# Optimization experiments

Measured on AMD Instinct MI355X. Metric: run time of the kernel, lower is better.

Reference implementation:

```python
import jax, jax.numpy as jnp
import numpy as np

NUM_EXPERTS = 8
TOP_K = 2


def setup_inputs() -> dict:
    key = jax.random.key(0)
    ks = jax.random.split(key, 5)
    B, S, H, F, E = 2, 2048, 1024, 4096, NUM_EXPERTS
    return {
        "hidden_states": jax.random.normal(ks[0], (B, S, H), dtype=jnp.float32),
        "router_w": jax.random.normal(ks[1], (H, E), dtype=jnp.float32) * 0.02,
        "router_b": jnp.zeros((E,), dtype=jnp.float32),
        "w1": jax.random.normal(ks[2], (E, H, F), dtype=jnp.float32) * 0.02,
        "b1": jnp.zeros((E, F), dtype=jnp.float32),
        "w2": jax.random.normal(ks[3], (E, F, H), dtype=jnp.float32) * 0.02,
        "b2": jnp.zeros((E, H), dtype=jnp.float32),
    }


def reference(hidden_states, router_w, router_b, w1, b1, w2, b2):
    # Router: softmax over experts, take top-2, renormalize.
    logits = jnp.einsum("bsh,he->bse", hidden_states, router_w) + router_b
    probs = jax.nn.softmax(logits, axis=-1)
    top_w, top_i = jax.lax.top_k(probs, TOP_K)              # [B,S,2]
    top_w = top_w / jnp.sum(top_w, axis=-1, keepdims=True)
    # Combine weights per expert: [B,S,E] (sum of slot weights where routed).
    combine = jnp.sum(
        top_w[..., None] * jax.nn.one_hot(top_i, NUM_EXPERTS, dtype=top_w.dtype),
        axis=-2,
    )
    # Dense expert FFN over stacked experts (grouped GEMM form).
    h = jax.nn.gelu(
        jnp.einsum("bsh,ehf->ebsf", hidden_states, w1) + b1[:, None, None, :],
        approximate=False,
    )  # exact GELU matches torch nn.GELU default
    y = jnp.einsum("ebsf,efh->ebsh", h, w2) + b2[:, None, None, :]
    # Weighted combine of top-2 expert outputs per token.
    return jnp.einsum("bse,ebsh->bsh", combine, y)
```

## Files before the change

kernel.cpp:

```cpp
#include <hip/hip_runtime.h>
#include <hip/hip_bf16.h>
#include <stdint.h>

#define T_TOKENS 4096
#define H_DIM    1024
#define F_DIM    4096
#define NE       8
#define NA       8192

typedef __bf16 bf16x8 __attribute__((ext_vector_type(8)));
typedef float  f32x4  __attribute__((ext_vector_type(4)));

__device__ __forceinline__ float b2f(unsigned short u) {
    union { float f; uint32_t i; } v; v.i = ((uint32_t)u) << 16; return v.f;
}
__device__ __forceinline__ unsigned short f2b(float f) {
    union { float f; uint32_t i; } v; v.f = f;
    uint32_t x = v.i;
    return (unsigned short)((x + 0x7FFFu + ((x >> 16) & 1u)) >> 16);
}

__device__ __forceinline__ void gl_lds16(const void* g, void* l) {
    __builtin_amdgcn_global_load_lds(
        (const __attribute__((address_space(1))) void*)g,
        (__attribute__((address_space(3))) void*)l,
        16, 0, 0);
}

__global__ void probe_kernel(const unsigned short* __restrict__ hs,
                             int* __restrict__ flag) {
    int lane = threadIdx.x;
    int cnt = 0;
    for (int j = 0; j < 16; j++) {
        unsigned short u = hs[(lane * 16 + j) * 2];
        int e = (u >> 7) & 0xFF;
        if (e >= 100 && e <= 135) cnt++;
    }
    for (int off = 32; off > 0; off >>= 1) cnt += __shfl_down(cnt, off);
    if (lane == 0) *flag = (cnt >= 512) ? 0 : 1;
}

__global__ __launch_bounds__(256) void router_kernel(
    const void* __restrict__ hs, const void* __restrict__ rw,
    const void* __restrict__ rb, const int* __restrict__ flag,
    int* __restrict__ top_i, float* __restrict__ top_w,
    unsigned short* __restrict__ hsb) {
    bool f32 = (*flag != 0);
    int wave = threadIdx.x >> 6, lane = threadIdx.x & 63;
    int t = blockIdx.x * 4 + wave;
    unsigned short* hout = hsb + (size_t)t * H_DIM;
    float acc[NE];
#pragma unroll
    for (int e = 0; e < NE; e++) acc[e] = 0.f;
    if (f32) {
        const float* hrow = (const float*)hs + (size_t)t * H_DIM;
        const float* rwf = (const float*)rw;
        for (int j = 0; j < 16; j++) {
            int k = j * 64 + lane;
            float h = hrow[k];
            hout[k] = f2b(h);
            float4 a = *(const float4*)(rwf + (size_t)k * NE);
            float4 b = *(const float4*)(rwf + (size_t)k * NE + 4);
            acc[0] += h * a.x; acc[1] += h * a.y; acc[2] += h * a.z; acc[3] += h * a.w;
            acc[4] += h * b.x; acc[5] += h * b.y; acc[6] += h * b.z; acc[7] += h * b.w;
        }
    } else {
        const unsigned short* hrow = (const unsigned short*)hs + (size_t)t * H_DIM;
        const unsigned short* rwu = (const unsigned short*)rw;
        for (int j = 0; j < 16; j++) {
            int k = j * 64 + lane;
            unsigned short hu = hrow[k];
            hout[k] = hu;
            float h = b2f(hu);
            uint4 rv = *(const uint4*)(rwu + (size_t)k * NE);
            const unsigned short* rs = (const unsigned short*)&rv;
#pragma unroll
            for (int e = 0; e < NE; e++) acc[e] += h * b2f(rs[e]);
        }
    }
#pragma unroll
    for (int e = 0; e < NE; e++)
        for (int off = 32; off > 0; off >>= 1) acc[e] += __shfl_down(acc[e], off);
    if (lane == 0) {
        float lg[NE];
#pragma unroll
        for (int e = 0; e < NE; e++)
            lg[e] = acc[e] + (f32 ? ((const float*)rb)[e]
                                  : b2f(((const unsigned short*)rb)[e]));
        int e0 = 0;
        for (int e = 1; e < NE; e++) if (lg[e] > lg[e0]) e0 = e;
        int e1 = (e0 == 0) ? 1 : 0;
        for (int e = 0; e < NE; e++) if (e != e0 && lg[e] > lg[e1]) e1 = e;
        float w0 = 1.f / (1.f + expf(lg[e1] - lg[e0]));
        top_i[t * 2] = e0; top_i[t * 2 + 1] = e1;
        top_w[t * 2] = w0; top_w[t * 2 + 1] = 1.f - w0;
    }
}

__global__ __launch_bounds__(256) void assign_kernel(
    const int* __restrict__ top_i, const float* __restrict__ top_w,
    int* __restrict__ token_list, float* __restrict__ wgt_list,
    int* __restrict__ assign_row, int* __restrict__ counts,
    int* __restrict__ offsets) {
    __shared__ int cnt_s[NE], cur_s[NE];
    int tid = threadIdx.x;
    if (tid < NE) cnt_s[tid] = 0;
    __syncthreads();
    for (int idx = tid; idx < NA; idx += 256) atomicAdd(&cnt_s[top_i[idx]], 1);
    __syncthreads();
    if (tid == 0) {
        int run = 0;
        for (int e = 0; e < NE; e++) {
            offsets[e] = run; counts[e] = cnt_s[e]; cur_s[e] = run; run += cnt_s[e];
        }
    }
    __syncthreads();
    for (int idx = tid; idx < NA; idx += 256) {
        int e = top_i[idx];
        int pos = atomicAdd(&cur_s[e], 1);
        token_list[pos] = idx >> 1;
        wgt_list[pos] = top_w[idx];
        assign_row[idx] = pos;
    }
}

__global__ __launch_bounds__(256) void transpose_kernel(
    const void* __restrict__ in, unsigned short* __restrict__ out,
    int R, int C, const int* __restrict__ flag) {
    bool f32 = (*flag != 0);
    size_t zo = (size_t)blockIdx.z * R * C;
    int c0 = blockIdx.x * 64, r0 = blockIdx.y * 64;
    __shared__ unsigned short t[64][65];
    int tx = threadIdx.x & 31, ty = threadIdx.x >> 5;
    if (f32) {
        const float* inf = (const float*)in + zo;
#pragma unroll
        for (int i = 0; i < 8; i++) {
            int r = ty + i * 8;
            float2 v = *(const float2*)&inf[(size_t)(r0 + r) * C + c0 + tx * 2];
            t[r][tx * 2] = f2b(v.x); t[r][tx * 2 + 1] = f2b(v.y);
        }
    } else {
        const unsigned short* inu = (const unsigned short*)in + zo;
#pragma unroll
        for (int i = 0; i < 8; i++) {
            int r = ty + i * 8;
            ushort2 v = *(const ushort2*)&inu[(size_t)(r0 + r) * C + c0 + tx * 2];
            t[r][tx * 2] = v.x; t[r][tx * 2 + 1] = v.y;
        }
    }
    __syncthreads();
#pragma unroll
    for (int i = 0; i < 8; i++) {
        int cc = ty + i * 8;
        ushort2 w; w.x = t[tx * 2][cc]; w.y = t[tx * 2 + 1][cc];
        *(ushort2*)&out[zo + (size_t)(c0 + cc) * R + r0 + tx * 2] = w;
    }
}

template <int MODE>
__global__ __launch_bounds__(256) void gemm_kernel(
    const unsigned short* __restrict__ Abase,
    const unsigned short* __restrict__ Bt,
    const void* __restrict__ bias,
    const int* __restrict__ flag,
    const int* __restrict__ token_list, const float* __restrict__ wgt_list,
    const int* __restrict__ counts, const int* __restrict__ offsets,
    unsigned short* __restrict__ act_out, unsigned short* __restrict__ y_out) {
    constexpr int K    = (MODE == 0) ? H_DIM : F_DIM;
    constexpr int NDIM = (MODE == 0) ? F_DIM : H_DIM;
    constexpr int AST  = (MODE == 0) ? H_DIM : F_DIM;
    constexpr int BM   = (MODE == 0) ? 128 : 64;
    constexpr int MI   = BM / 32;

    const int e = blockIdx.z;
    const int cnt = counts[e];
    const int m0 = blockIdx.y * BM;
    if (m0 >= cnt) return;
    const int off = offsets[e];
    const int n0 = blockIdx.x * 128;
    const bool f32 = (*flag != 0);

    __shared__ __bf16 As[BM * 64];
    __shared__ __bf16 Bs[128 * 64];
    __shared__ int   tok_s[BM];
    __shared__ float wgt_s[BM];

    const int tid = threadIdx.x;
    const int wave = tid >> 6, lane = tid & 63;

    if (tid < BM) {
        int r = off + min(m0 + tid, cnt - 1);
        tok_s[tid] = (MODE == 0) ? token_list[r] : r;
        wgt_s[tid] = wgt_list[r];
    }
    __syncthreads();

    const char* Abytes = (const char*)Abase;
    const char* Bbytes = (const char*)(Bt + (size_t)e * NDIM * K);
    uint64_t ga[MI], gb[4];
    const int chunk = (lane & 7) ^ ((lane >> 3) & 7);
#pragma unroll
    for (int i = 0; i < MI; i++) {
        int rowA = (wave * MI + i) * 8 + (lane >> 3);
        int arow = tok_s[rowA];
        ga[i] = (uint64_t)(uintptr_t)(Abytes + ((size_t)arow * AST + chunk * 8) * 2);
    }
#pragma unroll
    for (int i = 0; i < 4; i++) {
        int rowB = n0 + (wave * 4 + i) * 8 + (lane >> 3);
        gb[i] = (uint64_t)(uintptr_t)(Bbytes + ((size_t)rowB * K + chunk * 8) * 2);
    }

    f32x4 acc[MI][4];
#pragma unroll
    for (int i = 0; i < MI; i++)
#pragma unroll
        for (int j = 0; j < 4; j++) acc[i][j] = (f32x4){0.f, 0.f, 0.f, 0.f};

    const int wr = wave >> 1, wc = wave & 1;
    const int lane15 = lane & 15, quad = lane >> 4;

    for (int kt = 0; kt < K / 64; kt++) {
#pragma unroll
        for (int i = 0; i < MI; i++) {
            gl_lds16((const void*)(uintptr_t)ga[i], (void*)(As + (wave * MI + i) * 512));
            ga[i] += 128;
        }
#pragma unroll
        for (int i = 0; i < 4; i++) {
            gl_lds16((const void*)(uintptr_t)gb[i], (void*)(Bs + (wave * 4 + i) * 512));
            gb[i] += 128;
        }
        __syncthreads();
#pragma unroll
        for (int kk = 0; kk < 2; kk++) {
            bf16x8 a[MI], b[4];
#pragma unroll
            for (int i = 0; i < MI; i++) {
                int row = wr * (BM / 2) + i * 16 + lane15;
                int koff = (kk * 32 + quad * 8) ^ ((row & 7) * 8);
                a[i] = *(const bf16x8*)&As[row * 64 + koff];
            }
#pragma unroll
            for (int j = 0; j < 4; j++) {
                int row = wc * 64 + j * 16 + lane15;
                int koff = (kk * 32 + quad * 8) ^ ((row & 7) * 8);
                b[j] = *(const bf16x8*)&Bs[row * 64 + koff];
            }
#pragma unroll
            for (int i = 0; i < MI; i++)
#pragma unroll
                for (int j = 0; j < 4; j++)
                    acc[i][j] = __builtin_amdgcn_mfma_f32_16x16x32_bf16(a[i], b[j], acc[i][j], 0, 0, 0);
        }
        __syncthreads();
    }

#pragma unroll
    for (int j = 0; j < 4; j++) {
        int col = n0 + wc * 64 + j * 16 + lane15;
        float bv = f32 ? ((const float*)bias)[(size_t)e * NDIM + col]
                       : b2f(((const unsigned short*)bias)[(size_t)e * NDIM + col]);
#pragma unroll
        for (int i = 0; i < MI; i++) {
#pragma unroll
            for (int r = 0; r < 4; r++) {
                int rowl = wr * (BM / 2) + i * 16 + quad * 4 + r;
                if (m0 + rowl < cnt) {
                    float v = acc[i][j][r] + bv;
                    if (MODE == 0) {
                        v = 0.5f * v * (1.f + erff(v * 0.70710678118f));
                        act_out[(size_t)(off + m0 + rowl) * F_DIM + col] = f2b(v);
                    } else {
                        y_out[(size_t)(off + m0 + rowl) * H_DIM + col] = f2b(v * wgt_s[rowl]);
                    }
                }
            }
        }
    }
}

__global__ __launch_bounds__(256) void combine_kernel(
    const unsigned short* __restrict__ y, const int* __restrict__ assign_row,
    void* __restrict__ out, const int* __restrict__ flag) {
    bool f32 = (*flag != 0);
    int t = blockIdx.x;
    int r0 = assign_row[t * 2], r1 = assign_row[t * 2 + 1];
    ushort4 a = ((const ushort4*)(y + (size_t)r0 * H_DIM))[threadIdx.x];
    ushort4 b = ((const ushort4*)(y + (size_t)r1 * H_DIM))[threadIdx.x];
    float s0 = b2f(a.x) + b2f(b.x), s1 = b2f(a.y) + b2f(b.y);
    float s2 = b2f(a.z) + b2f(b.z), s3 = b2f(a.w) + b2f(b.w);
    if (f32) {
        float4 o = {s0, s1, s2, s3};
        ((float4*)out)[(size_t)t * (H_DIM / 4) + threadIdx.x] = o;
    } else {
        ushort4 o;
        o.x = f2b(s0); o.y = f2b(s1); o.z = f2b(s2); o.w = f2b(s3);
        ((ushort4*)((unsigned short*)out + (size_t)t * H_DIM))[threadIdx.x] = o;
    }
}

extern "C" void kernel_launch(void* const* d_in, const int* in_sizes, int n_in,
                              void* d_out, int out_size, void* d_ws, size_t ws_size,
                              hipStream_t stream) {
    const void* hs = d_in[0];
    const void* rw = d_in[1];
    const void* rb = d_in[2];
    const void* w1 = d_in[3];
    const void* b1 = d_in[4];
    const void* w2 = d_in[5];
    const void* b2 = d_in[6];

    char* ws = (char*)d_ws;
    size_t o = 0;
    auto alloc = [&](size_t bytes) {
        char* p = ws + o; o += (bytes + 255) & ~(size_t)255; return p;
    };
    unsigned short* wt   = (unsigned short*)alloc((size_t)NE * F_DIM * H_DIM * 2);
    unsigned short* act  = (unsigned short*)alloc((size_t)NA * F_DIM * 2);
    unsigned short* yb   = (unsigned short*)alloc((size_t)NA * H_DIM * 2);
    unsigned short* hsb  = (unsigned short*)alloc((size_t)T_TOKENS * H_DIM * 2);
    int*   top_i      = (int*)alloc(NA * 4);
    float* top_w      = (float*)alloc(NA * 4);
    int*   token_list = (int*)alloc(NA * 4);
    float* wgt_list   = (float*)alloc(NA * 4);
    int*   assign_row = (int*)alloc(NA * 4);
    int*   counts     = (int*)alloc(64);
    int*   offsets    = (int*)alloc(64);
    int*   flag       = (int*)alloc(64);
    (void)ws_size; (void)in_sizes; (void)n_in; (void)out_size;

    probe_kernel<<<1, 64, 0, stream>>>((const unsigned short*)hs, flag);
    router_kernel<<<T_TOKENS / 4, 256, 0, stream>>>(hs, rw, rb, flag, top_i, top_w, hsb);
    assign_kernel<<<1, 256, 0, stream>>>(top_i, top_w, token_list, wgt_list,
                                         assign_row, counts, offsets);
    transpose_kernel<<<dim3(F_DIM / 64, H_DIM / 64, NE), 256, 0, stream>>>(
        w1, wt, H_DIM, F_DIM, flag);
    gemm_kernel<0><<<dim3(F_DIM / 128, T_TOKENS / 128, NE), 256, 0, stream>>>(
        hsb, wt, b1, flag, token_list, wgt_list, counts, offsets, act, nullptr);
    transpose_kernel<<<dim3(H_DIM / 64, F_DIM / 64, NE), 256, 0, stream>>>(
        w2, wt, F_DIM, H_DIM, flag);
    gemm_kernel<1><<<dim3(H_DIM / 128, NA / 64, NE), 256, 0, stream>>>(
        act, wt, b2, flag, token_list, wgt_list, counts, offsets, nullptr, yb);
    combine_kernel<<<T_TOKENS, 256, 0, stream>>>(yb, assign_row, d_out, flag);
}
```

Before: 666.4 us.

## Double-buffer GEMM LDS tiles, vectorize transpose, approximate GELU, shrink grid

```diff
diff --git a/kernel.cpp b/kernel.cpp
--- a/kernel.cpp
+++ b/kernel.cpp
@@ -18,6 +18,16 @@
     union { float f; uint32_t i; } v; v.f = f;
     uint32_t x = v.i;
     return (unsigned short)((x + 0x7FFFu + ((x >> 16) & 1u)) >> 16);
+}
+
+__device__ __forceinline__ float gelu_f(float x) {
+    float z = fabsf(x) * 0.70710678118f;
+    float t = 1.0f / (1.0f + 0.3275911f * z);
+    float p = t * (0.254829592f + t * (-0.284496736f +
+              t * (1.421413741f + t * (-1.453152027f + t * 1.061405429f))));
+    float erf_z = 1.0f - p * __expf(-z * z);
+    float sgn_erf = (x >= 0.f) ? erf_z : -erf_z;
+    return x * (0.5f + 0.5f * sgn_erf);
 }
 
 __device__ __forceinline__ void gl_lds16(const void* g, void* l) {
@@ -131,30 +141,34 @@
     size_t zo = (size_t)blockIdx.z * R * C;
     int c0 = blockIdx.x * 64, r0 = blockIdx.y * 64;
     __shared__ unsigned short t[64][65];
-    int tx = threadIdx.x & 31, ty = threadIdx.x >> 5;
+    int tx = threadIdx.x & 15, ty = threadIdx.x >> 4;
     if (f32) {
         const float* inf = (const float*)in + zo;
 #pragma unroll
-        for (int i = 0; i < 8; i++) {
-            int r = ty + i * 8;
-            float2 v = *(const float2*)&inf[(size_t)(r0 + r) * C + c0 + tx * 2];
-            t[r][tx * 2] = f2b(v.x); t[r][tx * 2 + 1] = f2b(v.y);
+        for (int i = 0; i < 4; i++) {
+            int r = ty + i * 16;
+            float4 v = *(const float4*)&inf[(size_t)(r0 + r) * C + c0 + tx * 4];
+            t[r][tx * 4] = f2b(v.x); t[r][tx * 4 + 1] = f2b(v.y);
+            t[r][tx * 4 + 2] = f2b(v.z); t[r][tx * 4 + 3] = f2b(v.w);
         }
     } else {
         const unsigned short* inu = (const unsigned short*)in + zo;
 #pragma unroll
-        for (int i = 0; i < 8; i++) {
-            int r = ty + i * 8;
-            ushort2 v = *(const ushort2*)&inu[(size_t)(r0 + r) * C + c0 + tx * 2];
-            t[r][tx * 2] = v.x; t[r][tx * 2 + 1] = v.y;
-        }
-    }
-    __syncthreads();
-#pragma unroll
-    for (int i = 0; i < 8; i++) {
-        int cc = ty + i * 8;
-        ushort2 w; w.x = t[tx * 2][cc]; w.y = t[tx * 2 + 1][cc];
-        *(ushort2*)&out[zo + (size_t)(c0 + cc) * R + r0 + tx * 2] = w;
+        for (int i = 0; i < 4; i++) {
+            int r = ty + i * 16;
+            ushort4 v = *(const ushort4*)&inu[(size_t)(r0 + r) * C + c0 + tx * 4];
+            t[r][tx * 4] = v.x; t[r][tx * 4 + 1] = v.y;
+            t[r][tx * 4 + 2] = v.z; t[r][tx * 4 + 3] = v.w;
+        }
+    }
+    __syncthreads();
+#pragma unroll
+    for (int i = 0; i < 4; i++) {
+        int cc = ty + i * 16;
+        ushort4 w;
+        w.x = t[tx * 4][cc]; w.y = t[tx * 4 + 1][cc];
+        w.z = t[tx * 4 + 2][cc]; w.w = t[tx * 4 + 3][cc];
+        *(ushort4*)&out[zo + (size_t)(c0 + cc) * R + r0 + tx * 4] = w;
     }
 }
 
@@ -172,6 +186,10 @@
     constexpr int AST  = (MODE == 0) ? H_DIM : F_DIM;
     constexpr int BM   = (MODE == 0) ? 128 : 64;
     constexpr int MI   = BM / 32;
+    constexpr int NIA  = BM / 64;
+    constexpr int NK   = K / 32;
+    constexpr int ABUF = BM * 32;
+    constexpr int BBUF = 128 * 32;
 
     const int e = blockIdx.z;
     const int cnt = counts[e];
@@ -181,8 +199,8 @@
     const int n0 = blockIdx.x * 128;
     const bool f32 = (*flag != 0);
 
-    __shared__ __bf16 As[BM * 64];
-    __shared__ __bf16 Bs[128 * 64];
+    __shared__ __bf16 As[2 * ABUF];
+    __shared__ __bf16 Bs[2 * BBUF];
     __shared__ int   tok_s[BM];
     __shared__ float wgt_s[BM];
 
@@ -198,18 +216,21 @@
 
     const char* Abytes = (const char*)Abase;
     const char* Bbytes = (const char*)(Bt + (size_t)e * NDIM * K);
-    uint64_t ga[MI], gb[4];
-    const int chunk = (lane & 7) ^ ((lane >> 3) & 7);
-#pragma unroll
-    for (int i = 0; i < MI; i++) {
-        int rowA = (wave * MI + i) * 8 + (lane >> 3);
-        int arow = tok_s[rowA];
-        ga[i] = (uint64_t)(uintptr_t)(Abytes + ((size_t)arow * AST + chunk * 8) * 2);
-    }
-#pragma unroll
-    for (int i = 0; i < 4; i++) {
-        int rowB = n0 + (wave * 4 + i) * 8 + (lane >> 3);
-        gb[i] = (uint64_t)(uintptr_t)(Bbytes + ((size_t)rowB * K + chunk * 8) * 2);
+    const int rl = lane >> 2;
+    const int chk = (lane & 3) ^ (rl & 3);
+    uint64_t ga[NIA], gb[2];
+    uint32_t la[NIA], lb[2];
+#pragma unroll
+    for (int j = 0; j < NIA; j++) {
+        int rowA = (wave * NIA + j) * 16 + rl;
+        ga[j] = (uint64_t)(uintptr_t)(Abytes + ((size_t)tok_s[rowA] * AST + chk * 8) * 2);
+        la[j] = (wave * NIA + j) * 512;
+    }
+#pragma unroll
+    for (int j = 0; j < 2; j++) {
+        int rowB = n0 + (wave * 2 + j) * 16 + rl;
+        gb[j] = (uint64_t)(uintptr_t)(Bbytes + ((size_t)rowB * K + chk * 8) * 2);
+        lb[j] = (wave * 2 + j) * 512;
     }
 
     f32x4 acc[MI][4];
@@ -221,39 +242,51 @@
     const int wr = wave >> 1, wc = wave & 1;
     const int lane15 = lane & 15, quad = lane >> 4;
 
-    for (int kt = 0; kt < K / 64; kt++) {
+#pragma unroll
+    for (int j = 0; j < NIA; j++) {
+        gl_lds16((const void*)(uintptr_t)ga[j], (void*)(As + la[j]));
+        ga[j] += 64;
+    }
+#pragma unroll
+    for (int j = 0; j < 2; j++) {
+        gl_lds16((const void*)(uintptr_t)gb[j], (void*)(Bs + lb[j]));
+        gb[j] += 64;
+    }
+    __syncthreads();
+
+    for (int kt = 0; kt < NK; kt++) {
+        const int cur = kt & 1;
+        if (kt + 1 < NK) {
+            const int nxt = cur ^ 1;
+#pragma unroll
+            for (int j = 0; j < NIA; j++) {
+                gl_lds16((const void*)(uintptr_t)ga[j], (void*)(As + nxt * ABUF + la[j]));
+                ga[j] += 64;
+            }
+#pragma unroll
+            for (int j = 0; j < 2; j++) {
+                gl_lds16((const void*)(uintptr_t)gb[j], (void*)(Bs + nxt * BBUF + lb[j]));
+                gb[j] += 64;
+            }
+        }
+        const __bf16* Ab = As + cur * ABUF;
+        const __bf16* Bb = Bs + cur * BBUF;
+        bf16x8 a[MI], b[4];
 #pragma unroll
         for (int i = 0; i < MI; i++) {
-            gl_lds16((const void*)(uintptr_t)ga[i], (void*)(As + (wave * MI + i) * 512));
-            ga[i] += 128;
-        }
-#pragma unroll
-        for (int i = 0; i < 4; i++) {
-            gl_lds16((const void*)(uintptr_t)gb[i], (void*)(Bs + (wave * 4 + i) * 512));
-            gb[i] += 128;
-        }
-        __syncthreads();
-#pragma unroll
-        for (int kk = 0; kk < 2; kk++) {
-            bf16x8 a[MI], b[4];
-#pragma unroll
-            for (int i = 0; i < MI; i++) {
-                int row = wr * (BM / 2) + i * 16 + lane15;
-                int koff = (kk * 32 + quad * 8) ^ ((row & 7) * 8);
-                a[i] = *(const bf16x8*)&As[row * 64 + koff];
-            }
-#pragma unroll
-            for (int j = 0; j < 4; j++) {
-                int row = wc * 64 + j * 16 + lane15;
-                int koff = (kk * 32 + quad * 8) ^ ((row & 7) * 8);
-                b[j] = *(const bf16x8*)&Bs[row * 64 + koff];
-            }
-#pragma unroll
-            for (int i = 0; i < MI; i++)
-#pragma unroll
-                for (int j = 0; j < 4; j++)
-                    acc[i][j] = __builtin_amdgcn_mfma_f32_16x16x32_bf16(a[i], b[j], acc[i][j], 0, 0, 0);
-        }
+            int row = wr * (BM / 2) + i * 16 + lane15;
+            a[i] = *(const bf16x8*)&Ab[row * 32 + ((quad ^ (row & 3)) * 8)];
+        }
+#pragma unroll
+        for (int j = 0; j < 4; j++) {
+            int row = wc * 64 + j * 16 + lane15;
+            b[j] = *(const bf16x8*)&Bb[row * 32 + ((quad ^ (row & 3)) * 8)];
+        }
+#pragma unroll
+        for (int i = 0; i < MI; i++)
+#pragma unroll
+            for (int j = 0; j < 4; j++)
+                acc[i][j] = __builtin_amdgcn_mfma_f32_16x16x32_bf16(a[i], b[j], acc[i][j], 0, 0, 0);
         __syncthreads();
     }
 
@@ -270,8 +303,7 @@
                 if (m0 + rowl < cnt) {
                     float v = acc[i][j][r] + bv;
                     if (MODE == 0) {
-                        v = 0.5f * v * (1.f + erff(v * 0.70710678118f));
-                        act_out[(size_t)(off + m0 + rowl) * F_DIM + col] = f2b(v);
+                        act_out[(size_t)(off + m0 + rowl) * F_DIM + col] = f2b(gelu_f(v));
                     } else {
                         y_out[(size_t)(off + m0 + rowl) * H_DIM + col] = f2b(v * wgt_s[rowl]);
                     }
@@ -341,7 +373,7 @@
         hsb, wt, b1, flag, token_list, wgt_list, counts, offsets, act, nullptr);
     transpose_kernel<<<dim3(H_DIM / 64, F_DIM / 64, NE), 256, 0, stream>>>(
         w2, wt, F_DIM, H_DIM, flag);
-    gemm_kernel<1><<<dim3(H_DIM / 128, NA / 64, NE), 256, 0, stream>>>(
+    gemm_kernel<1><<<dim3(H_DIM / 128, T_TOKENS / 64, NE), 256, 0, stream>>>(
         act, wt, b2, flag, token_list, wgt_list, counts, offsets, nullptr, yb);
     combine_kernel<<<T_TOKENS, 256, 0, stream>>>(yb, assign_row, d_out, flag);
 }
```

After: 653.7 us. About the same (-1.9%).
